# Kernel tuning notes

Hardware: AMD Instinct MI355X
Metric: run time of the kernel (lower is better)

## Reference

```python
import jax, jax.numpy as jnp
import numpy as np

DIM, N_HEADS, N_EXPERTS, TOP_K = 1024, 16, 8, 2
D_FF = 4 * DIM
HEAD_DIM = DIM // N_HEADS
EPS = 1e-5


def layer_norm(x, g, b):
    m = x.mean(-1, keepdims=True)
    v = ((x - m) ** 2).mean(-1, keepdims=True)
    return (x - m) / jnp.sqrt(v + EPS) * g + b


def setup_inputs() -> dict:
    key = jax.random.key(0)
    ks = jax.random.split(key, 16)
    B, T = 8, 1024
    s = 0.02
    inp = {
        'x': jax.random.normal(ks[0], (B, T, DIM), jnp.float32),
        'attention_mask': jnp.ones((B, T), jnp.int32),
        'Wq': jax.random.normal(ks[1], (DIM, DIM), jnp.float32) * s,
        'bq': jnp.zeros((DIM,), jnp.float32),
        'Wk': jax.random.normal(ks[2], (DIM, DIM), jnp.float32) * s,
        'bk': jnp.zeros((DIM,), jnp.float32),
        'Wv': jax.random.normal(ks[3], (DIM, DIM), jnp.float32) * s,
        'bv': jnp.zeros((DIM,), jnp.float32),
        'Wo': jax.random.normal(ks[4], (DIM, DIM), jnp.float32) * s,
        'bo': jnp.zeros((DIM,), jnp.float32),
        'g1': jnp.ones((DIM,), jnp.float32),
        'beta1': jnp.zeros((DIM,), jnp.float32),
        'router_w': jax.random.normal(ks[5], (DIM, N_EXPERTS), jnp.float32) * s,
        'router_b': jnp.zeros((N_EXPERTS,), jnp.float32),
        'W1': jax.random.normal(ks[6], (N_EXPERTS, DIM, D_FF), jnp.float32) * s,
        'B1': jnp.zeros((N_EXPERTS, D_FF), jnp.float32),
        'W2': jax.random.normal(ks[7], (N_EXPERTS, D_FF, DIM), jnp.float32) * s,
        'B2': jnp.zeros((N_EXPERTS, DIM), jnp.float32),
        'g2': jnp.ones((DIM,), jnp.float32),
        'beta2': jnp.zeros((DIM,), jnp.float32),
    }
    return inp


def reference(x, attention_mask, Wq, bq, Wk, bk, Wv, bv, Wo, bo, g1, beta1,
              router_w, router_b, W1, B1, W2, B2, g2, beta2):
    B, T, D = x.shape
    H, hd = N_HEADS, HEAD_DIM
    # ---- multi-head attention with causal + padding mask ----
    q = (x @ Wq + bq).reshape(B, T, H, hd).transpose(0, 2, 1, 3)  # [B,H,T,hd]
    k = (x @ Wk + bk).reshape(B, T, H, hd).transpose(0, 2, 1, 3)
    v = (x @ Wv + bv).reshape(B, T, H, hd).transpose(0, 2, 1, 3)
    scores = jnp.einsum('bhqd,bhkd->bhqk', q, k) / jnp.sqrt(jnp.float32(hd))
    causal = jnp.tril(jnp.ones((T, T), bool))[None, None]            # [1,1,T,T]
    mask = causal & (attention_mask[:, None, None, :] != 0)         # [B,1,T,T]
    scores = jnp.where(mask, scores, jnp.float32(-1e9))
    attn = jax.nn.softmax(scores, axis=-1)
    h = jnp.einsum('bhqk,bhkd->bhqd', attn, v).transpose(0, 2, 1, 3).reshape(B, T, D)
    h = h @ Wo + bo
    # dropout is identity in eval mode
    x1 = layer_norm(x + h, g1, beta1)
    # ---- sparse top-k MoE FFN ----
    xf = x1.reshape(-1, D)                                           # [N,D]
    logits = xf @ router_w + router_b                                # [N,E]
    probs = jax.nn.softmax(logits, axis=-1)
    topv, topi = jax.lax.top_k(probs, TOP_K)                         # [N,k]
    gk = topv / topv.sum(-1, keepdims=True)                          # renormalized gates
    onehot = jax.nn.one_hot(topi, N_EXPERTS, dtype=xf.dtype)         # [N,k,E]
    gates = (onehot * gk[..., None]).sum(1)                          # [N,E]
    y = jnp.zeros_like(xf)
    for e in range(N_EXPERTS):  # fixed small expert loop
        he = jax.nn.relu(xf @ W1[e] + B1[e])
        y = y + gates[:, e:e + 1] * (he @ W2[e] + B2[e])
    # load-balancing loss: E * sum_i f_i * P_i
    f = onehot.sum(1).mean(0)                                        # fraction routed per expert
    P = probs.mean(0)
    lb = jnp.float32(N_EXPERTS) * (f * P).sum()
    out = layer_norm(x1 + y.reshape(B, T, D), g2, beta2)
    return out, lb
```

## Files before the change

kernel.cpp:

```cpp
#include <hip/hip_runtime.h>
#include <hip/hip_bf16.h>
#include <stdint.h>

#define DIMQ   1024
#define NHEADS 16
#define HD     64
#define NEXP   8
#define DFF    4096
#define NTOK   8192
#define TSEQ   1024
#define BATCH  8

typedef unsigned short u16;
typedef unsigned int   u32;
typedef __attribute__((ext_vector_type(8))) short bf16x8;
typedef __attribute__((ext_vector_type(4))) float f32x4;

__device__ __forceinline__ float bf_lo(u32 w) { return __uint_as_float(w << 16); }
__device__ __forceinline__ float bf_hi(u32 w) { return __uint_as_float(w & 0xffff0000u); }
__device__ __forceinline__ u16 f2bf(float f) {
  u32 x = __float_as_uint(f);
  return (u16)((x + 0x7fffu + ((x >> 16) & 1u)) >> 16);
}

__global__ __launch_bounds__(256) void cvt_f32_bf16(const float* __restrict__ in,
                                                    u16* __restrict__ out, int n) {
  int i = (blockIdx.x * 256 + threadIdx.x) * 4;
  if (i >= n) return;
  float4 v = *(const float4*)(in + i);
  ushort4 o;
  o.x = f2bf(v.x); o.y = f2bf(v.y); o.z = f2bf(v.z); o.w = f2bf(v.w);
  *(ushort4*)(out + i) = o;
}

__global__ __launch_bounds__(256) void transpose_f32_bf16(
    const float* __restrict__ in, u16* __restrict__ out, int R, int C) {
  __shared__ float tile[32][33];
  size_t base = (size_t)blockIdx.z * (size_t)R * (size_t)C;
  int tx = threadIdx.x & 31, ty = threadIdx.x >> 5;
  int c = blockIdx.x * 32 + tx;
#pragma unroll
  for (int i = 0; i < 4; i++) {
    int r = blockIdx.y * 32 + ty + i * 8;
    tile[ty + i * 8][tx] = in[base + (size_t)r * C + c];
  }
  __syncthreads();
  int rr = blockIdx.y * 32 + tx;
#pragma unroll
  for (int i = 0; i < 4; i++) {
    int cc = blockIdx.x * 32 + ty + i * 8;
    out[base + (size_t)cc * R + rr] = f2bf(tile[tx][ty + i * 8]);
  }
}

template <bool GATHER, bool RELU, bool TRANSC>
__device__ __forceinline__ void gemm_core(
    const u16* __restrict__ A, const u16* __restrict__ Bt,
    const float* __restrict__ bias, u16* __restrict__ C,
    int M, int N, int K, const int* __restrict__ gidx) {
  __shared__ u16 As[128 * 32];
  __shared__ u16 Bs[128 * 32];
  const int tid = threadIdx.x;
  const int lane = tid & 63;
  const int wave = tid >> 6;
  const int wr = wave >> 1, wc = wave & 1;
  const int lr = lane & 15, kg = lane >> 4;
  const int rowbase = blockIdx.y * 128;
  const int colbase = blockIdx.x * 128;

  f32x4 acc[4][4];
#pragma unroll
  for (int m = 0; m < 4; m++)
#pragma unroll
    for (int n = 0; n < 4; n++) acc[m][n] = (f32x4){0.f, 0.f, 0.f, 0.f};

  const int r0 = tid >> 2, seg = tid & 3;
  long arow0 = -1, arow1 = -1;
  if (rowbase + r0 < M)      arow0 = GATHER ? gidx[rowbase + r0]      : (rowbase + r0);
  if (rowbase + r0 + 64 < M) arow1 = GATHER ? gidx[rowbase + r0 + 64] : (rowbase + r0 + 64);
  const u16* Brow0 = Bt + (size_t)(colbase + r0) * K + seg * 8;
  const u16* Brow1 = Bt + (size_t)(colbase + r0 + 64) * K + seg * 8;

  for (int k0 = 0; k0 < K; k0 += 32) {
    __syncthreads();
    uint4 a0 = {0, 0, 0, 0}, a1 = {0, 0, 0, 0};
    if (arow0 >= 0) a0 = *(const uint4*)(A + (size_t)arow0 * K + k0 + seg * 8);
    if (arow1 >= 0) a1 = *(const uint4*)(A + (size_t)arow1 * K + k0 + seg * 8);
    *(uint4*)(&As[r0 * 32 + seg * 8]) = a0;
    *(uint4*)(&As[(r0 + 64) * 32 + seg * 8]) = a1;
    *(uint4*)(&Bs[r0 * 32 + seg * 8]) = *(const uint4*)(Brow0 + k0);
    *(uint4*)(&Bs[(r0 + 64) * 32 + seg * 8]) = *(const uint4*)(Brow1 + k0);
    __syncthreads();
    bf16x8 af[4], bfr[4];
#pragma unroll
    for (int m = 0; m < 4; m++)
      af[m] = *(const bf16x8*)(&As[(wr * 64 + m * 16 + lr) * 32 + kg * 8]);
#pragma unroll
    for (int n = 0; n < 4; n++)
      bfr[n] = *(const bf16x8*)(&Bs[(wc * 64 + n * 16 + lr) * 32 + kg * 8]);
#pragma unroll
    for (int m = 0; m < 4; m++)
#pragma unroll
      for (int n = 0; n < 4; n++)
        acc[m][n] = __builtin_amdgcn_mfma_f32_16x16x32_bf16(af[m], bfr[n], acc[m][n], 0, 0, 0);
  }
#pragma unroll
  for (int n = 0; n < 4; n++) {
    int col = colbase + wc * 64 + n * 16 + lr;
    float bv = bias[col];
#pragma unroll
    for (int m = 0; m < 4; m++) {
      int row0 = rowbase + wr * 64 + m * 16 + kg * 4;
      if (TRANSC) {
        if (row0 + 3 < M) {
          ushort4 pk;
          pk.x = f2bf(acc[m][n][0] + bv);
          pk.y = f2bf(acc[m][n][1] + bv);
          pk.z = f2bf(acc[m][n][2] + bv);
          pk.w = f2bf(acc[m][n][3] + bv);
          *(ushort4*)(&C[(size_t)col * M + row0]) = pk;
        } else {
#pragma unroll
          for (int r = 0; r < 4; r++)
            if (row0 + r < M) C[(size_t)col * M + row0 + r] = f2bf(acc[m][n][r] + bv);
        }
      } else {
#pragma unroll
        for (int r = 0; r < 4; r++) {
          int row = row0 + r;
          if (row < M) {
            float v = acc[m][n][r] + bv;
            if (RELU) v = fmaxf(v, 0.f);
            C[(size_t)row * N + col] = f2bf(v);
          }
        }
      }
    }
  }
}

__global__ __launch_bounds__(256) void gemm_bt_kernel(
    const u16* __restrict__ A, const u16* __restrict__ Bt,
    const float* __restrict__ bias, u16* __restrict__ C, int M, int N, int K) {
  gemm_core<false, false, false>(A, Bt, bias, C, M, N, K, nullptr);
}

__global__ __launch_bounds__(256) void gemm_bt_tc_kernel(
    const u16* __restrict__ A, const u16* __restrict__ Bt,
    const float* __restrict__ bias, u16* __restrict__ C, int M, int N, int K) {
  gemm_core<false, false, true>(A, Bt, bias, C, M, N, K, nullptr);
}

__global__ __launch_bounds__(256) void moe_gemm1_kernel(
    const u16* __restrict__ x1b, const u16* __restrict__ W1t,
    const float* __restrict__ B1, u16* __restrict__ he,
    const int* __restrict__ cnt, const int* __restrict__ off,
    const int* __restrict__ idxlist) {
  int e = blockIdx.z;
  int M = cnt[e];
  if ((int)blockIdx.y * 128 >= M) return;
  gemm_core<true, true, false>(x1b, W1t + (size_t)e * DFF * DIMQ, B1 + e * DFF,
                               he + (size_t)off[e] * DFF, M, DFF, DIMQ, idxlist + off[e]);
}

__global__ __launch_bounds__(256) void moe_gemm2_kernel(
    const u16* __restrict__ he, const u16* __restrict__ W2t,
    const float* __restrict__ B2, u16* __restrict__ yslot,
    const int* __restrict__ cnt, const int* __restrict__ off) {
  int e = blockIdx.z;
  int M = cnt[e];
  if ((int)blockIdx.y * 128 >= M) return;
  gemm_core<false, false, false>(he + (size_t)off[e] * DFF, W2t + (size_t)e * DIMQ * DFF,
                                 B2 + e * DIMQ, yslot + (size_t)off[e] * DIMQ, M, DIMQ, DFF, nullptr);
}

__global__ __launch_bounds__(256) void attn_mfma_kernel(
    const u16* __restrict__ qb, const u16* __restrict__ kb,
    const u16* __restrict__ vbT, const int* __restrict__ amask,
    u16* __restrict__ hb) {
  __shared__ u16 Ks[32 * 64];
  __shared__ u16 VTs[64 * 32];
  __shared__ u16 Ps[4][16 * 32];
  __shared__ float mbias[32];

  const int b = blockIdx.y >> 4;
  const int h = blockIdx.y & 15;
  const int qb0 = blockIdx.x * 64;
  const int tid = threadIdx.x;
  const int lane = tid & 63;
  const int wq = tid >> 6;
  const int r16 = lane & 15;
  const int kg = lane >> 4;
  const int qrow0 = qb0 + wq * 16;

  bf16x8 qf[2];
  {
    const u16* qp = qb + ((size_t)(b * TSEQ + qrow0 + r16)) * DIMQ + h * HD + kg * 8;
    qf[0] = *(const bf16x8*)(qp);
    qf[1] = *(const bf16x8*)(qp + 32);
  }
  f32x4 acc[4];
#pragma unroll
  for (int db = 0; db < 4; db++) acc[db] = (f32x4){0.f, 0.f, 0.f, 0.f};
  float m_run[4], l_run[4];
#pragma unroll
  for (int i = 0; i < 4; i++) { m_run[i] = -3.0e38f; l_run[i] = 0.f; }

  const int skey = tid >> 3, sslot = tid & 7;
  const int sd = tid >> 2, sko = tid & 3;
  const u16* kgb = kb + (size_t)(b * TSEQ) * DIMQ + h * HD;
  const u16* vgb = vbT + (size_t)(h * HD) * NTOK + (size_t)b * TSEQ;

  const int nt = (qb0 + 64) >> 5;
  for (int kt = 0; kt < nt; kt++) {
    const int k0g = kt * 32;
    __syncthreads();
    {
      uint4 kv = *(const uint4*)(kgb + (size_t)(k0g + skey) * DIMQ + sslot * 8);
      *(uint4*)(&Ks[skey * 64 + ((sslot ^ (skey & 7)) * 8)]) = kv;
      uint4 vv = *(const uint4*)(vgb + (size_t)sd * NTOK + k0g + sko * 8);
      *(uint4*)(&VTs[sd * 32 + ((sko ^ (sd & 3)) * 8)]) = vv;
      if (tid < 32) mbias[tid] = amask[b * TSEQ + k0g + tid] ? 0.f : -1e9f;
    }
    __syncthreads();
    if (k0g < qrow0 + 16) {
      f32x4 s0 = (f32x4){0.f, 0.f, 0.f, 0.f};
      f32x4 s1 = (f32x4){0.f, 0.f, 0.f, 0.f};
      {
        int key0 = r16;
        bf16x8 ka = *(const bf16x8*)(&Ks[key0 * 64 + ((kg ^ (key0 & 7)) * 8)]);
        bf16x8 kb2 = *(const bf16x8*)(&Ks[key0 * 64 + (((4 + kg) ^ (key0 & 7)) * 8)]);
        s0 = __builtin_amdgcn_mfma_f32_16x16x32_bf16(qf[0], ka, s0, 0, 0, 0);
        s0 = __builtin_amdgcn_mfma_f32_16x16x32_bf16(qf[1], kb2, s0, 0, 0, 0);
        int key1 = 16 + r16;
        bf16x8 kc = *(const bf16x8*)(&Ks[key1 * 64 + ((kg ^ (key1 & 7)) * 8)]);
        bf16x8 kd = *(const bf16x8*)(&Ks[key1 * 64 + (((4 + kg) ^ (key1 & 7)) * 8)]);
        s1 = __builtin_amdgcn_mfma_f32_16x16x32_bf16(qf[0], kc, s1, 0, 0, 0);
        s1 = __builtin_amdgcn_mfma_f32_16x16x32_bf16(qf[1], kd, s1, 0, 0, 0);
      }
      float sv0[4], sv1[4], tm[4];
      float mb0 = mbias[r16], mb1 = mbias[16 + r16];
#pragma unroll
      for (int i = 0; i < 4; i++) {
        int qg = qrow0 + kg * 4 + i;
        float a = s0[i] * 0.125f + mb0;
        float c = s1[i] * 0.125f + mb1;
        if (k0g + r16 > qg)      a = -3.0e38f;
        if (k0g + 16 + r16 > qg) c = -3.0e38f;
        sv0[i] = a; sv1[i] = c;
        tm[i] = fmaxf(a, c);
      }
#pragma unroll
      for (int mk = 1; mk < 16; mk <<= 1) {
#pragma unroll
        for (int i = 0; i < 4; i++) tm[i] = fmaxf(tm[i], __shfl_xor(tm[i], mk));
      }
      float pr0[4], pr1[4];
#pragma unroll
      for (int i = 0; i < 4; i++) {
        float nm = fmaxf(m_run[i], tm[i]);
        float sc = __expf(m_run[i] - nm);
        m_run[i] = nm;
        pr0[i] = __expf(sv0[i] - nm);
        pr1[i] = __expf(sv1[i] - nm);
        l_run[i] = l_run[i] * sc + pr0[i] + pr1[i];
#pragma unroll
        for (int db = 0; db < 4; db++) acc[db][i] *= sc;
      }
#pragma unroll
      for (int i = 0; i < 4; i++) {
        int qrl = kg * 4 + i;
        int sw = qrl & 3;
        Ps[wq][qrl * 32 + (((r16 >> 3) ^ sw) * 8) + (r16 & 7)] = f2bf(pr0[i]);
        Ps[wq][qrl * 32 + ((((16 + r16) >> 3) ^ sw) * 8) + (r16 & 7)] = f2bf(pr1[i]);
      }
      bf16x8 pf = *(const bf16x8*)(&Ps[wq][r16 * 32 + ((kg ^ (r16 & 3)) * 8)]);
#pragma unroll
      for (int db = 0; db < 4; db++) {
        int d = db * 16 + r16;
        bf16x8 vf = *(const bf16x8*)(&VTs[d * 32 + ((kg ^ (d & 3)) * 8)]);
        acc[db] = __builtin_amdgcn_mfma_f32_16x16x32_bf16(pf, vf, acc[db], 0, 0, 0);
      }
    }
  }
#pragma unroll
  for (int mk = 1; mk < 16; mk <<= 1) {
#pragma unroll
    for (int i = 0; i < 4; i++) l_run[i] += __shfl_xor(l_run[i], mk);
  }
#pragma unroll
  for (int i = 0; i < 4; i++) {
    float inv = 1.f / l_run[i];
    int qg = qrow0 + kg * 4 + i;
    u16* op = hb + ((size_t)(b * TSEQ + qg)) * DIMQ + h * HD + r16;
#pragma unroll
    for (int db = 0; db < 4; db++) op[db * 16] = f2bf(acc[db][i] * inv);
  }
}

__global__ __launch_bounds__(256) void addln_kernel(
    const float* __restrict__ xin, const u16* __restrict__ hres,
    const float* __restrict__ g, const float* __restrict__ beta,
    float* __restrict__ x1, u16* __restrict__ x1b) {
  __shared__ float red[8];
  int t = blockIdx.x;
  int d = threadIdx.x * 4;
  size_t base = (size_t)t * DIMQ + d;
  float4 xv = *(const float4*)(xin + base);
  uint2 hu = *(const uint2*)(hres + base);
  float v0 = xv.x + bf_lo(hu.x), v1 = xv.y + bf_hi(hu.x);
  float v2 = xv.z + bf_lo(hu.y), v3 = xv.w + bf_hi(hu.y);
  float s1 = v0 + v1 + v2 + v3;
  float s2 = v0 * v0 + v1 * v1 + v2 * v2 + v3 * v3;
#pragma unroll
  for (int off = 32; off; off >>= 1) {
    s1 += __shfl_down(s1, off);
    s2 += __shfl_down(s2, off);
  }
  int w = threadIdx.x >> 6;
  if ((threadIdx.x & 63) == 0) { red[w] = s1; red[4 + w] = s2; }
  __syncthreads();
  float S1 = red[0] + red[1] + red[2] + red[3];
  float S2 = red[4] + red[5] + red[6] + red[7];
  float m = S1 * (1.f / DIMQ);
  float var = S2 * (1.f / DIMQ) - m * m;
  float rs = rsqrtf(var + 1e-5f);
  float4 gv = *(const float4*)(g + d);
  float4 bv = *(const float4*)(beta + d);
  float o0 = (v0 - m) * rs * gv.x + bv.x;
  float o1 = (v1 - m) * rs * gv.y + bv.y;
  float o2 = (v2 - m) * rs * gv.z + bv.z;
  float o3 = (v3 - m) * rs * gv.w + bv.w;
  *(float4*)(x1 + base) = make_float4(o0, o1, o2, o3);
  uint2 pu;
  pu.x = (u32)f2bf(o0) | ((u32)f2bf(o1) << 16);
  pu.y = (u32)f2bf(o2) | ((u32)f2bf(o3) << 16);
  *(uint2*)(x1b + base) = pu;
}

__global__ __launch_bounds__(256) void router_kernel(
    const float* __restrict__ x1, const float* __restrict__ rw,
    const float* __restrict__ rb, int* __restrict__ topi,
    float* __restrict__ gkout, float* __restrict__ probs) {
  int t = blockIdx.x * 4 + (threadIdx.x >> 6);
  int l = threadIdx.x & 63;
  float acc[8];
#pragma unroll
  for (int e = 0; e < 8; e++) acc[e] = 0.f;
  const float* xr = x1 + (size_t)t * DIMQ;
  for (int k = l; k < DIMQ; k += 64) {
    float xv = xr[k];
    const float* w = rw + (size_t)k * 8;
#pragma unroll
    for (int e = 0; e < 8; e++) acc[e] += xv * w[e];
  }
#pragma unroll
  for (int e = 0; e < 8; e++) {
#pragma unroll
    for (int off = 32; off; off >>= 1) acc[e] += __shfl_down(acc[e], off);
  }
  if (l == 0) {
    float lg[8], p[8];
    float mx = -3e38f;
#pragma unroll
    for (int e = 0; e < 8; e++) { lg[e] = acc[e] + rb[e]; mx = fmaxf(mx, lg[e]); }
    float sum = 0.f;
#pragma unroll
    for (int e = 0; e < 8; e++) { p[e] = expf(lg[e] - mx); sum += p[e]; }
    float isum = 1.f / sum;
#pragma unroll
    for (int e = 0; e < 8; e++) p[e] *= isum;
    int e0 = 0;
#pragma unroll
    for (int e = 1; e < 8; e++) if (p[e] > p[e0]) e0 = e;
    int e1 = (e0 == 0) ? 1 : 0;
#pragma unroll
    for (int e = 0; e < 8; e++) if (e != e0 && p[e] > p[e1]) e1 = e;
    float s2 = p[e0] + p[e1];
    topi[2 * t] = e0; topi[2 * t + 1] = e1;
    gkout[2 * t] = p[e0] / s2; gkout[2 * t + 1] = p[e1] / s2;
    float* pp = probs + (size_t)t * 8;
#pragma unroll
    for (int e = 0; e < 8; e++) pp[e] = p[e];
  }
}

__global__ __launch_bounds__(256) void stats_kernel(
    const float* __restrict__ probs, const int* __restrict__ topi,
    int* __restrict__ cnt, float* __restrict__ Psum) {
  __shared__ float sps[4][8];
  __shared__ int   slc[4][8];
  float ps[8];
  int lc[8];
#pragma unroll
  for (int e = 0; e < 8; e++) { ps[e] = 0.f; lc[e] = 0; }
  int t = blockIdx.x * 256 + threadIdx.x;
  {
    const float* p = probs + (size_t)t * 8;
#pragma unroll
    for (int e = 0; e < 8; e++) ps[e] += p[e];
    lc[topi[2 * t]]++;
    lc[topi[2 * t + 1]]++;
  }
#pragma unroll
  for (int e = 0; e < 8; e++) {
#pragma unroll
    for (int off = 32; off; off >>= 1) {
      ps[e] += __shfl_down(ps[e], off);
      lc[e] += __shfl_down(lc[e], off);
    }
  }
  int w = threadIdx.x >> 6;
  if ((threadIdx.x & 63) == 0) {
#pragma unroll
    for (int e = 0; e < 8; e++) { sps[w][e] = ps[e]; slc[w][e] = lc[e]; }
  }
  __syncthreads();
  if (threadIdx.x < 8) {
    float fp = sps[0][threadIdx.x] + sps[1][threadIdx.x] + sps[2][threadIdx.x] + sps[3][threadIdx.x];
    int   fc = slc[0][threadIdx.x] + slc[1][threadIdx.x] + slc[2][threadIdx.x] + slc[3][threadIdx.x];
    atomicAdd(&Psum[threadIdx.x], fp);
    atomicAdd(&cnt[threadIdx.x], fc);
  }
}

__global__ void offsets_kernel(const int* __restrict__ cnt, const float* __restrict__ Psum,
                               int* __restrict__ off, int* __restrict__ fill,
                               float* __restrict__ lb_out) {
  if (threadIdx.x == 0 && blockIdx.x == 0) {
    int o = 0;
    float lb = 0.f;
    for (int e = 0; e < NEXP; e++) {
      off[e] = o;
      fill[e] = o;
      o += cnt[e];
      lb += ((float)cnt[e] / (float)NTOK) * (Psum[e] / (float)NTOK);
    }
    lb_out[0] = (float)NEXP * lb;
  }
}

__global__ __launch_bounds__(256) void listbuild_kernel(
    const int* __restrict__ topi, int* fill, int* __restrict__ idxlist,
    int* __restrict__ posmap) {
  __shared__ int bcnt[8];
  __shared__ int base[8];
  __shared__ int bofs[8];
  int t = blockIdx.x * 256 + threadIdx.x;
  if (threadIdx.x < 8) { bcnt[threadIdx.x] = 0; bofs[threadIdx.x] = 0; }
  __syncthreads();
  int e0 = topi[2 * t], e1 = topi[2 * t + 1];
  atomicAdd(&bcnt[e0], 1);
  atomicAdd(&bcnt[e1], 1);
  __syncthreads();
  if (threadIdx.x < 8) base[threadIdx.x] = atomicAdd(&fill[threadIdx.x], bcnt[threadIdx.x]);
  __syncthreads();
  int s0 = base[e0] + atomicAdd(&bofs[e0], 1);
  idxlist[s0] = t;
  posmap[2 * t] = s0;
  int s1 = base[e1] + atomicAdd(&bofs[e1], 1);
  idxlist[s1] = t;
  posmap[2 * t + 1] = s1;
}

__global__ __launch_bounds__(256) void finalln_kernel(
    const float* __restrict__ x1, const u16* __restrict__ yslot,
    const int* __restrict__ posmap, const float* __restrict__ gkv,
    const float* __restrict__ g, const float* __restrict__ beta,
    float* __restrict__ out) {
  __shared__ float red[8];
  int t = blockIdx.x;
  int p0 = posmap[2 * t], p1 = posmap[2 * t + 1];
  float g0 = gkv[2 * t], g1 = gkv[2 * t + 1];
  int d = threadIdx.x * 4;
  size_t base = (size_t)t * DIMQ + d;
  float4 xv = *(const float4*)(x1 + base);
  uint2 y0 = *(const uint2*)(yslot + (size_t)p0 * DIMQ + d);
  uint2 y1 = *(const uint2*)(yslot + (size_t)p1 * DIMQ + d);
  float v0 = xv.x + g0 * bf_lo(y0.x) + g1 * bf_lo(y1.x);
  float v1 = xv.y + g0 * bf_hi(y0.x) + g1 * bf_hi(y1.x);
  float v2 = xv.z + g0 * bf_lo(y0.y) + g1 * bf_lo(y1.y);
  float v3 = xv.w + g0 * bf_hi(y0.y) + g1 * bf_hi(y1.y);
  float s1 = v0 + v1 + v2 + v3;
  float s2 = v0 * v0 + v1 * v1 + v2 * v2 + v3 * v3;
#pragma unroll
  for (int off = 32; off; off >>= 1) {
    s1 += __shfl_down(s1, off);
    s2 += __shfl_down(s2, off);
  }
  int w = threadIdx.x >> 6;
  if ((threadIdx.x & 63) == 0) { red[w] = s1; red[4 + w] = s2; }
  __syncthreads();
  float S1 = red[0] + red[1] + red[2] + red[3];
  float S2 = red[4] + red[5] + red[6] + red[7];
  float m = S1 * (1.f / DIMQ);
  float var = S2 * (1.f / DIMQ) - m * m;
  float rs = rsqrtf(var + 1e-5f);
  float4 gv = *(const float4*)(g + d);
  float4 bv = *(const float4*)(beta + d);
  float4 o;
  o.x = (v0 - m) * rs * gv.x + bv.x;
  o.y = (v1 - m) * rs * gv.y + bv.y;
  o.z = (v2 - m) * rs * gv.z + bv.z;
  o.w = (v3 - m) * rs * gv.w + bv.w;
  *(float4*)(out + base) = o;
}

extern "C" void kernel_launch(void* const* d_in, const int* in_sizes, int n_in,
                              void* d_out, int out_size, void* d_ws, size_t ws_size,
                              hipStream_t stream) {
  const float* x     = (const float*)d_in[0];
  const int*   amask = (const int*)d_in[1];
  const float* Wq    = (const float*)d_in[2];
  const float* bq    = (const float*)d_in[3];
  const float* Wk    = (const float*)d_in[4];
  const float* bk    = (const float*)d_in[5];
  const float* Wv    = (const float*)d_in[6];
  const float* bv    = (const float*)d_in[7];
  const float* Wo    = (const float*)d_in[8];
  const float* bo    = (const float*)d_in[9];
  const float* g1    = (const float*)d_in[10];
  const float* beta1 = (const float*)d_in[11];
  const float* rw    = (const float*)d_in[12];
  const float* rb    = (const float*)d_in[13];
  const float* W1    = (const float*)d_in[14];
  const float* B1    = (const float*)d_in[15];
  const float* W2    = (const float*)d_in[16];
  const float* B2    = (const float*)d_in[17];
  const float* g2    = (const float*)d_in[18];
  const float* beta2 = (const float*)d_in[19];
  float* out    = (float*)d_out;
  float* lb_out = out + (size_t)NTOK * DIMQ;

  char* ws = (char*)d_ws;
  size_t off_acc = 0;
  auto alloc = [&](size_t bytes) {
    void* p = ws + off_acc;
    off_acc += (bytes + 255) & ~(size_t)255;
    return p;
  };
  u16* xb    = (u16*)alloc((size_t)NTOK * DIMQ * 2);
  u16* qbuf  = (u16*)alloc((size_t)NTOK * DIMQ * 2);
  u16* kbuf  = (u16*)alloc((size_t)NTOK * DIMQ * 2);
  u16* vbufT = (u16*)alloc((size_t)NTOK * DIMQ * 2);
  u16* hb    = (u16*)alloc((size_t)NTOK * DIMQ * 2);
  u16* ho    = (u16*)alloc((size_t)NTOK * DIMQ * 2);
  float* x1  = (float*)alloc((size_t)NTOK * DIMQ * 4);
  u16* x1b   = (u16*)alloc((size_t)NTOK * DIMQ * 2);
  u16* Wqt   = (u16*)alloc((size_t)DIMQ * DIMQ * 2);
  u16* Wkt   = (u16*)alloc((size_t)DIMQ * DIMQ * 2);
  u16* Wvt   = (u16*)alloc((size_t)DIMQ * DIMQ * 2);
  u16* Wot   = (u16*)alloc((size_t)DIMQ * DIMQ * 2);
  u16* W1t   = (u16*)alloc((size_t)NEXP * DFF * DIMQ * 2);
  u16* W2t   = (u16*)alloc((size_t)NEXP * DIMQ * DFF * 2);
  u16* he    = (u16*)alloc((size_t)2 * NTOK * DFF * 2);
  u16* yslot = (u16*)alloc((size_t)2 * NTOK * DIMQ * 2);
  char* stats = (char*)alloc(4096);
  int*   cnt   = (int*)stats;
  float* Psum  = (float*)(stats + 32);
  int*   offp  = (int*)(stats + 64);
  int*   fill  = (int*)(stats + 96);
  int* topi    = (int*)alloc((size_t)NTOK * 2 * 4);
  float* gkbuf = (float*)alloc((size_t)NTOK * 2 * 4);
  int* posmap  = (int*)alloc((size_t)NTOK * 2 * 4);
  int* idxlist = (int*)alloc((size_t)NTOK * 2 * 4);
  float* probs = (float*)alloc((size_t)NTOK * 8 * 4);

  hipMemsetAsync(stats, 0, 64, stream);

  cvt_f32_bf16<<<NTOK * DIMQ / 1024, 256, 0, stream>>>(x, xb, NTOK * DIMQ);
  transpose_f32_bf16<<<dim3(DIMQ / 32, DIMQ / 32, 1), 256, 0, stream>>>(Wq, Wqt, DIMQ, DIMQ);
  transpose_f32_bf16<<<dim3(DIMQ / 32, DIMQ / 32, 1), 256, 0, stream>>>(Wk, Wkt, DIMQ, DIMQ);
  transpose_f32_bf16<<<dim3(DIMQ / 32, DIMQ / 32, 1), 256, 0, stream>>>(Wv, Wvt, DIMQ, DIMQ);
  transpose_f32_bf16<<<dim3(DIMQ / 32, DIMQ / 32, 1), 256, 0, stream>>>(Wo, Wot, DIMQ, DIMQ);
  transpose_f32_bf16<<<dim3(DFF / 32, DIMQ / 32, NEXP), 256, 0, stream>>>(W1, W1t, DIMQ, DFF);
  transpose_f32_bf16<<<dim3(DIMQ / 32, DFF / 32, NEXP), 256, 0, stream>>>(W2, W2t, DFF, DIMQ);

  dim3 gproj(DIMQ / 128, NTOK / 128);
  gemm_bt_kernel<<<gproj, 256, 0, stream>>>(xb, Wqt, bq, qbuf, NTOK, DIMQ, DIMQ);
  gemm_bt_kernel<<<gproj, 256, 0, stream>>>(xb, Wkt, bk, kbuf, NTOK, DIMQ, DIMQ);
  gemm_bt_tc_kernel<<<gproj, 256, 0, stream>>>(xb, Wvt, bv, vbufT, NTOK, DIMQ, DIMQ);
  attn_mfma_kernel<<<dim3(TSEQ / 64, BATCH * NHEADS), 256, 0, stream>>>(qbuf, kbuf, vbufT, amask, hb);
  gemm_bt_kernel<<<gproj, 256, 0, stream>>>(hb, Wot, bo, ho, NTOK, DIMQ, DIMQ);
  addln_kernel<<<NTOK, 256, 0, stream>>>(x, ho, g1, beta1, x1, x1b);

  router_kernel<<<NTOK / 4, 256, 0, stream>>>(x1, rw, rb, topi, gkbuf, probs);
  stats_kernel<<<NTOK / 256, 256, 0, stream>>>(probs, topi, cnt, Psum);
  offsets_kernel<<<1, 64, 0, stream>>>(cnt, Psum, offp, fill, lb_out);
  listbuild_kernel<<<NTOK / 256, 256, 0, stream>>>(topi, fill, idxlist, posmap);
  moe_gemm1_kernel<<<dim3(DFF / 128, NTOK / 128, NEXP), 256, 0, stream>>>(x1b, W1t, B1, he, cnt, offp, idxlist);
  moe_gemm2_kernel<<<dim3(DIMQ / 128, NTOK / 128, NEXP), 256, 0, stream>>>(he, W2t, B2, yslot, cnt, offp);
  finalln_kernel<<<NTOK, 256, 0, stream>>>(x1, yslot, posmap, gkbuf, g2, beta2, out);
}
```

Baseline: 989.6 us.

## Load GEMM tiles directly into LDS with XOR-swizzled layout

Replaces the register-staged global-to-LDS copy in the bf16 MFMA GEMM with global_load_lds direct transfers and applies an XOR swizzle on the k-segment to reduce LDS bank conflicts when fragments are read. Out-of-range A rows are clamped to the last valid row instead of being zero-filled, and the barrier moves to the end of the loop. This aims to cut VGPR traffic and LDS conflicts in the hot GEMM, at the cost of relying on LDS write ordering and on the clamped rows never being stored.

```diff
diff --git a/kernel.cpp b/kernel.cpp
--- a/kernel.cpp
+++ b/kernel.cpp
@@ -21,6 +21,11 @@
 __device__ __forceinline__ u16 f2bf(float f) {
   u32 x = __float_as_uint(f);
   return (u16)((x + 0x7fffu + ((x >> 16) & 1u)) >> 16);
+}
+
+__device__ __forceinline__ void gload16(const u16* g, u16* l) {
+  __builtin_amdgcn_global_load_lds((const __attribute__((address_space(1))) u32*)g,
+                                   (__attribute__((address_space(3))) u32*)l, 16, 0, 0);
 }
 
 __global__ __launch_bounds__(256) void cvt_f32_bf16(const float* __restrict__ in,
@@ -75,34 +80,41 @@
     for (int n = 0; n < 4; n++) acc[m][n] = (f32x4){0.f, 0.f, 0.f, 0.f};
 
   const int r0 = tid >> 2, seg = tid & 3;
-  long arow0 = -1, arow1 = -1;
-  if (rowbase + r0 < M)      arow0 = GATHER ? gidx[rowbase + r0]      : (rowbase + r0);
-  if (rowbase + r0 + 64 < M) arow1 = GATHER ? gidx[rowbase + r0 + 64] : (rowbase + r0 + 64);
-  const u16* Brow0 = Bt + (size_t)(colbase + r0) * K + seg * 8;
-  const u16* Brow1 = Bt + (size_t)(colbase + r0 + 64) * K + seg * 8;
+  const int slog = seg ^ ((r0 >> 1) & 3);
+  int ar0 = rowbase + r0;      if (ar0 >= M) ar0 = M - 1;
+  int ar1 = rowbase + r0 + 64; if (ar1 >= M) ar1 = M - 1;
+  const long arow0 = GATHER ? gidx[ar0] : ar0;
+  const long arow1 = GATHER ? gidx[ar1] : ar1;
+  const u16* Aptr0 = A + (size_t)arow0 * K + slog * 8;
+  const u16* Aptr1 = A + (size_t)arow1 * K + slog * 8;
+  const u16* Bptr0 = Bt + (size_t)(colbase + r0) * K + slog * 8;
+  const u16* Bptr1 = Bt + (size_t)(colbase + r0 + 64) * K + slog * 8;
+  u16* ldsA0 = &As[tid * 8];
+  u16* ldsA1 = &As[2048 + tid * 8];
+  u16* ldsB0 = &Bs[tid * 8];
+  u16* ldsB1 = &Bs[2048 + tid * 8];
+
+  const int swz = (lr >> 1) & 3;
 
   for (int k0 = 0; k0 < K; k0 += 32) {
-    __syncthreads();
-    uint4 a0 = {0, 0, 0, 0}, a1 = {0, 0, 0, 0};
-    if (arow0 >= 0) a0 = *(const uint4*)(A + (size_t)arow0 * K + k0 + seg * 8);
-    if (arow1 >= 0) a1 = *(const uint4*)(A + (size_t)arow1 * K + k0 + seg * 8);
-    *(uint4*)(&As[r0 * 32 + seg * 8]) = a0;
-    *(uint4*)(&As[(r0 + 64) * 32 + seg * 8]) = a1;
-    *(uint4*)(&Bs[r0 * 32 + seg * 8]) = *(const uint4*)(Brow0 + k0);
-    *(uint4*)(&Bs[(r0 + 64) * 32 + seg * 8]) = *(const uint4*)(Brow1 + k0);
+    gload16(Aptr0 + k0, ldsA0);
+    gload16(Aptr1 + k0, ldsA1);
+    gload16(Bptr0 + k0, ldsB0);
+    gload16(Bptr1 + k0, ldsB1);
     __syncthreads();
     bf16x8 af[4], bfr[4];
 #pragma unroll
     for (int m = 0; m < 4; m++)
-      af[m] = *(const bf16x8*)(&As[(wr * 64 + m * 16 + lr) * 32 + kg * 8]);
+      af[m] = *(const bf16x8*)(&As[(wr * 64 + m * 16 + lr) * 32 + ((kg ^ swz) * 8)]);
 #pragma unroll
     for (int n = 0; n < 4; n++)
-      bfr[n] = *(const bf16x8*)(&Bs[(wc * 64 + n * 16 + lr) * 32 + kg * 8]);
+      bfr[n] = *(const bf16x8*)(&Bs[(wc * 64 + n * 16 + lr) * 32 + ((kg ^ swz) * 8)]);
 #pragma unroll
     for (int m = 0; m < 4; m++)
 #pragma unroll
       for (int n = 0; n < 4; n++)
         acc[m][n] = __builtin_amdgcn_mfma_f32_16x16x32_bf16(af[m], bfr[n], acc[m][n], 0, 0, 0);
+    __syncthreads();
   }
 #pragma unroll
   for (int n = 0; n < 4; n++) {
```

Result: faster. 934.4 us (-5.6%).
